# Kernel optimization log

Hardware: AMD Instinct MI355X
Metric: run time of the kernel (lower is better)

The kernel has to match this reference:

```python
import jax, jax.numpy as jnp
import numpy as np

D = 16          # input_dim (no augmentations)
HID = 256       # hidden_dim
WIN = 64        # window_size
LEN = 1000      # len_noise
INTU = 50       # len_interval_u
B = 512
PAIRS = D * (D - 1) // 2      # 120 depth-2 Lyndon pairs
LOGSIG = D + PAIRS            # 136 logsignature channels


def _static_schedule():
    """Replicates compute_multilevel_logsignature's index logic on static times."""
    tb = np.linspace(0.0, 1.0, LEN)
    tu = tb[::INTU]
    tt = np.linspace(0.0, 1.0, WIN)
    u_indices = np.searchsorted(tb, tu, side='right') - 1
    t_indices = np.searchsorted(tb, tt[1:], side='right') - 1
    u_idx_for_t = np.searchsorted(tu, tt[1:], side='right') - 1
    start_idx = u_indices[np.maximum(u_idx_for_t, 0)]
    # build u_logsigrnn times and the per-step last_h update mask
    qt, last = [], -1
    for iu in u_idx_for_t:
        iu = max(int(iu), 0)
        if iu != last:
            qt.append(tu[iu]); last = iu
    qt.append(tt[-1])
    upd = np.zeros(WIN, dtype=bool)
    for i, t in enumerate(tt):
        if qt and t >= qt[0]:
            qt.pop(0); upd[i] = True
    return tb, t_indices, start_idx, upd


def setup_inputs() -> dict:
    key = jax.random.key(0)
    ks = jax.random.split(key, 6)
    def lin(k, fo, fi):  # kaiming-style fan_in init
        return jax.random.normal(k, (fo, fi), jnp.float32) * np.float32(np.sqrt(2.0 / fi))
    return {
        "z": jax.random.normal(ks[0], (B, LEN, D), jnp.float32),
        "W1": lin(ks[1], HID, HID + LOGSIG), "b1": jnp.zeros((HID,), jnp.float32),
        "W2": lin(ks[2], HID, HID),          "b2": jnp.zeros((HID,), jnp.float32),
        "W3": lin(ks[3], HID, HID),          "b3": jnp.zeros((HID,), jnp.float32),
        "W_lin": lin(ks[4], HID, HID),
    }


def reference(z, W1, b1, W2, b2, W3, b3, W_lin):
    tb, t_idx, s_idx, upd = _static_schedule()
    # Brownian path: z[:,0]=0, z[:,1:] *= sqrt(dt), cumsum
    dt_sqrt = jnp.sqrt(jnp.asarray(np.diff(tb), jnp.float32))          # [LEN-1]
    z = jnp.concatenate([jnp.zeros_like(z[:, :1]), z[:, 1:] * dt_sqrt[None, :, None]], axis=1)
    X = jnp.cumsum(z, axis=1)                                           # [B,LEN,D]
    # depth-2 logsignature with basepoint=0: level1 = X[end]; level2 = Levy area
    iu, ju = np.triu_indices(D, 1)
    Xp, dX = X[:, :-1], X[:, 1:] - X[:, :-1]
    pair = Xp[..., iu] * dX[..., ju] - Xp[..., ju] * dX[..., iu]        # [B,LEN-1,PAIRS]
    C = jnp.concatenate([jnp.zeros_like(pair[:, :1]), jnp.cumsum(pair, axis=1)], axis=1)
    lvl1 = X[:, t_idx]
    levy = 0.5 * (C[:, t_idx] - C[:, s_idx])
    logsig = jnp.concatenate([lvl1, levy], axis=-1)
    logsig = jnp.concatenate([jnp.zeros_like(logsig[:, :1]), logsig], axis=1)  # prepend zeros
    seq = jnp.moveaxis(logsig, 1, 0)

    def mlp(v):  # FeedForwardNN([hid,hid]) + Tanh
        v = jax.nn.relu(v @ W1.T + b1)
        v = jax.nn.relu(v @ W2.T + b2)
        return jnp.tanh(v @ W3.T + b3)

    def step(last_h, xs):
        ls, u = xs
        h = mlp(jnp.concatenate([last_h, ls], axis=-1))
        new_last = jnp.where(u, h, last_h)
        return new_last, h @ W_lin.T

    h0 = jnp.zeros((z.shape[0], HID), z.dtype)  # init_fixed=True
    _, ys = jax.lax.scan(step, h0, (seq, jnp.asarray(upd)))
    return jnp.moveaxis(ys, 0, 1)
```

## Files before the change

### kernel.cpp

```cpp
#include <hip/hip_runtime.h>
#include <hip/hip_bf16.h>
#include <cmath>
#include <cstring>

#define B_SZ   512
#define SLEN   1000
#define DD     16
#define HID    256
#define WIN    64
#define PAIRS  120
#define LSIG   136
#define NWIN   20
#define MAXST  21
#define K1P    416
#define W1FN   (13 * 16 * 64 * 8)
#define WFN    (8 * 16 * 64 * 8)
#define PSTEP  21

using short8  = __attribute__((ext_vector_type(8))) short;
using short4v = __attribute__((ext_vector_type(4))) short;
using half8   = __attribute__((ext_vector_type(8))) _Float16;
using f32x4   = __attribute__((ext_vector_type(4))) float;

struct SchedArgs { short snapk[SLEN - 1]; };
struct CombPArgs { unsigned char winofm[WIN]; unsigned char zl[WIN]; unsigned char sstep[WIN]; };
struct ChainArgs { int nsteps; unsigned char kU[32]; };
struct FuseArgs  { unsigned char sidx[WIN]; };

__device__ __forceinline__ unsigned short f2h(float x) {
  _Float16 h = (_Float16)x;
  return __builtin_bit_cast(unsigned short, h);
}
__device__ __forceinline__ float ftanh(float x) {
  float t = fminf(fmaxf(2.f * x, -30.f), 30.f);
  float e = __expf(t);
  return (e - 1.f) / (e + 1.f);
}

__global__ __launch_bounds__(128) void prep_kernel(
    const float* __restrict__ z,
    const float* __restrict__ W1, const float* __restrict__ W2,
    const float* __restrict__ W3, const float* __restrict__ Wl,
    float* __restrict__ logsig, float* __restrict__ dxwin,
    unsigned short* __restrict__ W1f, unsigned short* __restrict__ W2f,
    unsigned short* __restrict__ W3f, unsigned short* __restrict__ Wlf,
    SchedArgs A)
{
  const int w = blockIdx.x, b = blockIdx.y, tid = threadIdx.x;
  if (w >= NWIN) {
    const int slot = ((w - NWIN) * B_SZ + b) * 128 + tid;
    for (int e = slot; e < W1FN + 3 * WFN; e += 3 * B_SZ * 128) {
      if (e < W1FN) {
        int f = e;
        int j = f & 7, l15 = (f >> 3) & 15, lq = (f >> 7) & 3, nsub = (f >> 9) & 15, kk = f >> 13;
        int row = nsub * 16 + l15, col = kk * 32 + lq * 8 + j;
        float v = (col < HID + LSIG) ? W1[(size_t)row * (HID + LSIG) + col] : 0.f;
        W1f[f] = f2h(v);
      } else {
        int e2 = e - W1FN;
        int which = e2 >> 16, f = e2 & 65535;
        int j = f & 7, l15 = (f >> 3) & 15, lq = (f >> 7) & 3, nsub = (f >> 9) & 15, kk = (f >> 13) & 7;
        int row = nsub * 16 + l15, col = kk * 32 + lq * 8 + j;
        const float* src = which == 0 ? W2 : which == 1 ? W3 : Wl;
        unsigned short* dst = which == 0 ? W2f : which == 1 ? W3f : Wlf;
        dst[f] = f2h(src[(size_t)row * HID + col]);
      }
    }
    return;
  }
  __shared__ float zs[50][16];
  const int ns = (w == NWIN - 1) ? 49 : 50;
  const float* src = z + ((size_t)b * SLEN + 50 * w + 1) * DD;
  const double s999 = 1.0 / (double)(SLEN - 1);
  for (int c = tid; c < ns * 4; c += 128) {
    float4 v = ((const float4*)src)[c];
    int t = 50 * w + (c >> 2);
    double a = (t + 1 == SLEN - 1) ? 1.0 : (double)(t + 1) * s999;
    float s = sqrtf((float)(a - (double)t * s999));
    v.x *= s; v.y *= s; v.z *= s; v.w *= s;
    ((float4*)&zs[0][0])[c] = v;
  }
  int pi = 0, pj = 0;
  if (tid < PAIRS) { int rem = tid, i = 0; while (rem >= DD - 1 - i) { rem -= DD - 1 - i; ++i; } pi = i; pj = i + 1 + rem; }
  __syncthreads();
  float Yi = 0.f, Yj = 0.f, LL = 0.f, Yd = 0.f;
  const int base_t = 50 * w;
  for (int u = 0; u < ns; ++u) {
    const float di = zs[u][pi], dj = zs[u][pj];
    LL = fmaf(Yi, dj, LL); LL = fmaf(-Yj, di, LL);
    Yi += di; Yj += dj;
    if (tid < DD) Yd += zs[u][tid];
    const int m = A.snapk[base_t + u];
    if (m) {
      float* dst = logsig + ((size_t)b * WIN + m) * LSIG;
      if (tid < DD)    dst[tid]      = Yd;
      if (tid < PAIRS) dst[DD + tid] = LL;
    }
  }
  if (tid < DD) dxwin[((size_t)b * NWIN + w) * DD + tid] = Yd;
}

__global__ __launch_bounds__(256) void combp_kernel(
    float* __restrict__ logsig, const float* __restrict__ dxwin,
    const unsigned short* __restrict__ W1f, const float* __restrict__ b1,
    float* __restrict__ partial, CombPArgs A)
{
  __shared__ float Xs[16][16], Yt[16][16];
  __shared__ __align__(16) unsigned short As[20 * 16 * 8];
  const int k = blockIdx.x, g = blockIdx.y, tid = threadIdx.x;
  const int w = A.winofm[k], zl = A.zl[k], ss = A.sstep[k];
  for (int c = tid; c < 3 * 16 * 8; c += 256) As[17 * 16 * 8 + c] = 0;
  {
    const int bi = tid >> 4, col = tid & 15;
    const size_t b = (size_t)(g * 16 + bi);
    float acc = 0.f;
    for (int ww = 0; ww < w; ++ww) acc += dxwin[(b * NWIN + ww) * DD + col];
    float y = (k == 0) ? 0.f : logsig[(b * WIN + k) * LSIG + col];
    float fin = (k == 0) ? 0.f : acc + y;
    Xs[bi][col] = acc; Yt[bi][col] = y;
    logsig[(b * WIN + k) * LSIG + col] = fin;
    As[((col >> 3) * 16 + bi) * 8 + (col & 7)] = f2h(fin);
  }
  __syncthreads();
  for (int idx = tid; idx < 16 * PAIRS; idx += 256) {
    const int bi = idx / PAIRS, p = idx - bi * PAIRS;
    int rem = p, i = 0; while (rem >= DD - 1 - i) { rem -= DD - 1 - i; ++i; }
    const int pi = i, pj = i + 1 + rem;
    const size_t b = (size_t)(g * 16 + bi);
    float ll = (k == 0) ? 0.f : logsig[(b * WIN + k) * LSIG + DD + p];
    float fin = (k == 0 || zl) ? 0.f
              : 0.5f * (ll + Xs[bi][pi] * Yt[bi][pj] - Xs[bi][pj] * Yt[bi][pi]);
    logsig[(b * WIN + k) * LSIG + DD + p] = fin;
    const int c = DD + p;
    As[((c >> 3) * 16 + bi) * 8 + (c & 7)] = f2h(fin);
  }
  if (ss == 255) return;
  __syncthreads();
  const int lane = tid & 63, wv = tid >> 6;
  const int l15 = lane & 15, lq = lane >> 4;
  f32x4 acc4[4] = {{0,0,0,0},{0,0,0,0},{0,0,0,0},{0,0,0,0}};
#pragma unroll
  for (int kt = 0; kt < 5; ++kt) {
    half8 af = *(const half8*)&As[((kt * 4 + lq) * 16 + l15) * 8];
#pragma unroll
    for (int t = 0; t < 4; ++t) {
      half8 bfW = *(const half8*)(W1f + ((size_t)((8 + kt) * 16 + wv * 4 + t) * 64 + lane) * 8);
      acc4[t] = __builtin_amdgcn_mfma_f32_16x16x32_f16(bfW, af, acc4[t], 0, 0, 0);
    }
  }
#pragma unroll
  for (int t = 0; t < 4; ++t) {
    const int col0 = wv * 64 + t * 16 + lq * 4;
    f32x4 bb = *(const f32x4*)(b1 + col0);
    f32x4 r = acc4[t] + bb;
    *(f32x4*)&partial[(((size_t)g * PSTEP + ss) * 16 + l15) * HID + col0] = r;
  }
}

__global__ __attribute__((amdgpu_flat_work_group_size(512, 512)))
__attribute__((amdgpu_waves_per_eu(2, 2)))
void chain_kernel(
    const float* __restrict__ partial,
    const unsigned short* __restrict__ W1f, const unsigned short* __restrict__ W2f,
    const unsigned short* __restrict__ W3f,
    const float* __restrict__ b2, const float* __restrict__ b3,
    unsigned short* __restrict__ statesb, ChainArgs A)
{
  __shared__ __align__(16) unsigned short A0s[32 * 16 * 8];
  __shared__ __align__(16) unsigned short A1s[32 * 16 * 8];
  __shared__ __align__(16) unsigned short A2s[32 * 16 * 8];
  const int tid = threadIdx.x, g = blockIdx.x;
  const int lane = tid & 63, w = tid >> 6;
  const int l15 = lane & 15, lq = lane >> 4;

  for (int c = tid; c < 32 * 16 * 8; c += 512) A0s[c] = 0;
  for (int c = tid; c < 16 * HID; c += 512) {
    int r = c >> 8, col = c & 255;
    statesb[((size_t)(g * 16 + r) * MAXST + 0) * HID + col] = 0;
  }

  half8 W1r[16], W2r[16], W3r[16];
#pragma unroll
  for (int kk = 0; kk < 8; ++kk)
#pragma unroll
    for (int nt = 0; nt < 2; ++nt) {
      W1r[kk * 2 + nt] = *(const half8*)(W1f + ((size_t)(kk * 16 + w * 2 + nt) * 64 + lane) * 8);
      W2r[kk * 2 + nt] = *(const half8*)(W2f + ((size_t)(kk * 16 + w * 2 + nt) * 64 + lane) * 8);
      W3r[kk * 2 + nt] = *(const half8*)(W3f + ((size_t)(kk * 16 + w * 2 + nt) * 64 + lane) * 8);
    }

  int colb[2];
  f32x4 bias2v[2], bias3v[2];
#pragma unroll
  for (int nt = 0; nt < 2; ++nt) {
    colb[nt] = w * 32 + nt * 16 + lq * 4;
    bias2v[nt] = *(const f32x4*)(b2 + colb[nt]);
    bias3v[nt] = *(const f32x4*)(b3 + colb[nt]);
  }

  const float* pbase = partial + (size_t)g * PSTEP * 16 * HID;
  int poff[2];
#pragma unroll
  for (int nt = 0; nt < 2; ++nt) poff[nt] = l15 * HID + colb[nt];
  f32x4 pf[2];
  pf[0] = *(const f32x4*)(pbase + poff[0]);
  pf[1] = *(const f32x4*)(pbase + poff[1]);

  short4v hv4[2];
  __syncthreads();

  for (int m = 0; m < A.nsteps; ++m) {
    if (m > 0) {
#pragma unroll
      for (int nt = 0; nt < 2; ++nt)
        *(short4v*)&statesb[((size_t)(g * 16 + l15) * MAXST + m) * HID + colb[nt]] = hv4[nt];
    }
    {
      f32x4 acc[2][2];
      acc[0][0] = pf[0]; acc[0][1] = pf[1];
      acc[1][0] = (f32x4){0.f,0.f,0.f,0.f}; acc[1][1] = (f32x4){0.f,0.f,0.f,0.f};
      if (m + 1 < A.nsteps) {
        const float* pp = pbase + (size_t)(m + 1) * 16 * HID;
        pf[0] = *(const f32x4*)(pp + poff[0]);
        pf[1] = *(const f32x4*)(pp + poff[1]);
      }
#pragma unroll
      for (int kk = 0; kk < 8; ++kk) {
        half8 af = *(const half8*)&A0s[((kk * 4 + lq) * 16 + l15) * 8];
        acc[kk & 1][0] = __builtin_amdgcn_mfma_f32_16x16x32_f16(W1r[kk * 2    ], af, acc[kk & 1][0], 0, 0, 0);
        acc[kk & 1][1] = __builtin_amdgcn_mfma_f32_16x16x32_f16(W1r[kk * 2 + 1], af, acc[kk & 1][1], 0, 0, 0);
      }
#pragma unroll
      for (int nt = 0; nt < 2; ++nt) {
        f32x4 s = acc[0][nt] + acc[1][nt];
        short4v h4;
#pragma unroll
        for (int r4 = 0; r4 < 4; ++r4) h4[r4] = (short)f2h(fmaxf(s[r4], 0.f));
        *(short4v*)&A1s[((colb[nt] >> 3) * 16 + l15) * 8 + (colb[nt] & 7)] = h4;
      }
    }
    __syncthreads();
    {
      f32x4 acc[2][2] = {{{0.f,0.f,0.f,0.f},{0.f,0.f,0.f,0.f}},{{0.f,0.f,0.f,0.f},{0.f,0.f,0.f,0.f}}};
#pragma unroll
      for (int kk = 0; kk < 8; ++kk) {
        half8 af = *(const half8*)&A1s[((kk * 4 + lq) * 16 + l15) * 8];
        acc[kk & 1][0] = __builtin_amdgcn_mfma_f32_16x16x32_f16(W2r[kk * 2    ], af, acc[kk & 1][0], 0, 0, 0);
        acc[kk & 1][1] = __builtin_amdgcn_mfma_f32_16x16x32_f16(W2r[kk * 2 + 1], af, acc[kk & 1][1], 0, 0, 0);
      }
#pragma unroll
      for (int nt = 0; nt < 2; ++nt) {
        f32x4 s = acc[0][nt] + acc[1][nt] + bias2v[nt];
        short4v h4;
#pragma unroll
        for (int r4 = 0; r4 < 4; ++r4) h4[r4] = (short)f2h(fmaxf(s[r4], 0.f));
        *(short4v*)&A2s[((colb[nt] >> 3) * 16 + l15) * 8 + (colb[nt] & 7)] = h4;
      }
    }
    __syncthreads();
    {
      f32x4 acc[2][2] = {{{0.f,0.f,0.f,0.f},{0.f,0.f,0.f,0.f}},{{0.f,0.f,0.f,0.f},{0.f,0.f,0.f,0.f}}};
#pragma unroll
      for (int kk = 0; kk < 8; ++kk) {
        half8 af = *(const half8*)&A2s[((kk * 4 + lq) * 16 + l15) * 8];
        acc[kk & 1][0] = __builtin_amdgcn_mfma_f32_16x16x32_f16(W3r[kk * 2    ], af, acc[kk & 1][0], 0, 0, 0);
        acc[kk & 1][1] = __builtin_amdgcn_mfma_f32_16x16x32_f16(W3r[kk * 2 + 1], af, acc[kk & 1][1], 0, 0, 0);
      }
#pragma unroll
      for (int nt = 0; nt < 2; ++nt) {
        f32x4 s = acc[0][nt] + acc[1][nt] + bias3v[nt];
        short4v h4;
#pragma unroll
        for (int r4 = 0; r4 < 4; ++r4) h4[r4] = (short)f2h(ftanh(s[r4]));
        hv4[nt] = h4;
        *(short4v*)&A0s[((colb[nt] >> 3) * 16 + l15) * 8 + (colb[nt] & 7)] = h4;
      }
    }
    __syncthreads();
  }
  {
    const int m = A.nsteps;
#pragma unroll
    for (int nt = 0; nt < 2; ++nt)
      *(short4v*)&statesb[((size_t)(g * 16 + l15) * MAXST + m) * HID + colb[nt]] = hv4[nt];
  }
}

__global__ __launch_bounds__(256, 4) void fused_kernel(
    const unsigned short* __restrict__ statesb, const float* __restrict__ logsig,
    const unsigned short* __restrict__ W1f, const unsigned short* __restrict__ W2f,
    const unsigned short* __restrict__ W3f, const unsigned short* __restrict__ Wlf,
    const float* __restrict__ b1, const float* __restrict__ b2, const float* __restrict__ b3,
    float* __restrict__ out, FuseArgs F)
{
  __shared__ __align__(16) unsigned short act[32 * 32 * 8];
  __shared__ __align__(16) unsigned short atile[2][4 * 32 * 8];
  const int tid = threadIdx.x;
  const int b = blockIdx.x >> 1, half = blockIdx.x & 1;
  const int lane = tid & 63, w = tid >> 6;
  const int l15 = lane & 15, lq = lane >> 4;

  f32x4 acc[2][4];
#pragma unroll
  for (int a = 0; a < 2; ++a)
#pragma unroll
    for (int t = 0; t < 4; ++t) acc[a][t] = (f32x4){0.f, 0.f, 0.f, 0.f};

  const int lr = tid >> 3, lcc = (tid & 7) * 4;
  const int lks = half * 32 + lr;
  short4v pk;
  auto loadA = [&](int kk) {
    int col = kk * 32 + lcc;
    if (col < HID) {
      pk = *(const short4v*)(statesb + ((size_t)b * MAXST + F.sidx[lks]) * HID + col);
    } else {
      const float* sp = logsig + ((size_t)b * WIN + lks) * LSIG + (col - HID);
      float4 v = *(const float4*)sp;
      short4v q;
      q[0] = (short)f2h(v.x); q[1] = (short)f2h(v.y); q[2] = (short)f2h(v.z); q[3] = (short)f2h(v.w);
      pk = q;
    }
  };
  loadA(0);
  for (int kk = 0; kk < 13; ++kk) {
    unsigned short* buf = &atile[kk & 1][0];
    *(short4v*)&buf[((lcc >> 3) * 32 + lr) * 8 + (lcc & 7)] = pk;
    __syncthreads();
    if (kk + 1 < 13) loadA(kk + 1);
    half8 bfr[4];
#pragma unroll
    for (int t = 0; t < 4; ++t)
      bfr[t] = *(const half8*)(W1f + ((size_t)(kk * 16 + w * 4 + t) * 64 + lane) * 8);
#pragma unroll
    for (int a = 0; a < 2; ++a) {
      half8 af = *(const half8*)&buf[(lq * 32 + a * 16 + l15) * 8];
#pragma unroll
      for (int t = 0; t < 4; ++t)
        acc[a][t] = __builtin_amdgcn_mfma_f32_16x16x32_f16(bfr[t], af, acc[a][t], 0, 0, 0);
    }
  }
#pragma unroll
  for (int t = 0; t < 4; ++t) {
    const int col0 = w * 64 + t * 16 + lq * 4;
    f32x4 bb = *(const f32x4*)(b1 + col0);
#pragma unroll
    for (int a = 0; a < 2; ++a) {
      const int row = a * 16 + l15;
      short4v h4;
#pragma unroll
      for (int r4 = 0; r4 < 4; ++r4) h4[r4] = (short)f2h(fmaxf(acc[a][t][r4] + bb[r4], 0.f));
      *(short4v*)&act[((col0 >> 3) * 32 + row) * 8 + (col0 & 7)] = h4;
    }
  }
  __syncthreads();

  auto layer = [&](const unsigned short* Wf) {
#pragma unroll
    for (int a = 0; a < 2; ++a)
#pragma unroll
      for (int t = 0; t < 4; ++t) acc[a][t] = (f32x4){0.f, 0.f, 0.f, 0.f};
    for (int kk = 0; kk < 8; ++kk) {
      half8 bfr[4];
#pragma unroll
      for (int t = 0; t < 4; ++t)
        bfr[t] = *(const half8*)(Wf + ((size_t)(kk * 16 + w * 4 + t) * 64 + lane) * 8);
#pragma unroll
      for (int a = 0; a < 2; ++a) {
        half8 af = *(const half8*)&act[((kk * 4 + lq) * 32 + a * 16 + l15) * 8];
#pragma unroll
        for (int t = 0; t < 4; ++t)
          acc[a][t] = __builtin_amdgcn_mfma_f32_16x16x32_f16(bfr[t], af, acc[a][t], 0, 0, 0);
      }
    }
  };

  layer(W2f);
  __syncthreads();
#pragma unroll
  for (int t = 0; t < 4; ++t) {
    const int col0 = w * 64 + t * 16 + lq * 4;
    f32x4 bb = *(const f32x4*)(b2 + col0);
#pragma unroll
    for (int a = 0; a < 2; ++a) {
      const int row = a * 16 + l15;
      short4v h4;
#pragma unroll
      for (int r4 = 0; r4 < 4; ++r4) h4[r4] = (short)f2h(fmaxf(acc[a][t][r4] + bb[r4], 0.f));
      *(short4v*)&act[((col0 >> 3) * 32 + row) * 8 + (col0 & 7)] = h4;
    }
  }
  __syncthreads();

  layer(W3f);
  __syncthreads();
#pragma unroll
  for (int t = 0; t < 4; ++t) {
    const int col0 = w * 64 + t * 16 + lq * 4;
    f32x4 bb = *(const f32x4*)(b3 + col0);
#pragma unroll
    for (int a = 0; a < 2; ++a) {
      const int row = a * 16 + l15;
      short4v h4;
#pragma unroll
      for (int r4 = 0; r4 < 4; ++r4) h4[r4] = (short)f2h(ftanh(acc[a][t][r4] + bb[r4]));
      *(short4v*)&act[((col0 >> 3) * 32 + row) * 8 + (col0 & 7)] = h4;
    }
  }
  __syncthreads();

  layer(Wlf);
#pragma unroll
  for (int t = 0; t < 4; ++t) {
    const int col0 = w * 64 + t * 16 + lq * 4;
#pragma unroll
    for (int a = 0; a < 2; ++a) {
      const int ks = half * 32 + a * 16 + l15;
      *(f32x4*)&out[((size_t)b * WIN + ks) * HID + col0] = acc[a][t];
    }
  }
}

static void build_sched(SchedArgs& P, CombPArgs& CB, ChainArgs& CH, FuseArgs& FU) {
  double tb[SLEN], tt[WIN], tu[NWIN];
  const double s999 = 1.0 / (double)(SLEN - 1);
  const double s63  = 1.0 / (double)(WIN - 1);
  for (int i = 0; i < SLEN; ++i) tb[i] = (double)i * s999;
  tb[SLEN - 1] = 1.0;
  for (int k = 0; k < WIN; ++k) tt[k] = (double)k * s63;
  tt[WIN - 1] = 1.0;
  for (int j = 0; j < NWIN; ++j) tu[j] = tb[50 * j];

  int t_idx[WIN - 1], u_for_t[WIN - 1];
  for (int k = 1; k < WIN; ++k) {
    int ii = 0;
    for (int q = 0; q < SLEN; ++q) if (tb[q] <= tt[k]) ii = q;
    t_idx[k - 1] = ii;
    int jj = 0;
    for (int q = 0; q < NWIN; ++q) if (tu[q] <= tt[k]) jj = q;
    u_for_t[k - 1] = jj;
  }
  for (int t = 0; t < SLEN - 1; ++t) P.snapk[t] = 0;
  for (int m = 1; m < WIN; ++m) P.snapk[t_idx[m - 1] - 1] = (short)m;

  for (int m = 0; m < WIN; ++m) { CB.winofm[m] = 0; CB.zl[m] = 0; CB.sstep[m] = 255; }
  for (int m = 1; m < WIN; ++m) {
    int p = t_idx[m - 1];
    CB.winofm[m] = (unsigned char)((p - 1) / 50);
    CB.zl[m] = (p % 50 == 0) ? 1 : 0;
  }

  double qt[32]; int nq = 0, last = -1;
  for (int m = 0; m < WIN - 1; ++m) {
    const int iu = u_for_t[m];
    if (iu != last) { qt[nq++] = tu[iu]; last = iu; }
  }
  qt[nq++] = tt[WIN - 1];
  int upd[WIN]; int qh = 0;
  for (int i = 0; i < WIN; ++i) {
    upd[i] = 0;
    if (qh < nq && tt[i] >= qt[qh]) { qh++; upd[i] = 1; }
  }
  int nU = 0;
  for (int k = 0; k < WIN; ++k) if (upd[k]) { if (nU < 32) CH.kU[nU] = (unsigned char)k; ++nU; }
  int cnt = 0;
  for (int k = 0; k < WIN; ++k) { FU.sidx[k] = (unsigned char)cnt; if (upd[k]) ++cnt; }
  CH.nsteps = FU.sidx[WIN - 1];
  for (int s = 0; s < nU && s < 32; ++s)
    if (s < PSTEP) CB.sstep[CH.kU[s]] = (unsigned char)s;
}

extern "C" void kernel_launch(void* const* d_in, const int* in_sizes, int n_in,
                              void* d_out, int out_size, void* d_ws, size_t ws_size,
                              hipStream_t stream) {
  const float* z  = (const float*)d_in[0];
  const float* W1 = (const float*)d_in[1];
  const float* b1 = (const float*)d_in[2];
  const float* W2 = (const float*)d_in[3];
  const float* b2 = (const float*)d_in[4];
  const float* W3 = (const float*)d_in[5];
  const float* b3 = (const float*)d_in[6];
  const float* Wl = (const float*)d_in[7];

  char* ws = (char*)d_ws;
  float* logsig = (float*)(ws);
  size_t o = (size_t)B_SZ * WIN * LSIG * 4;
  float* dxwin            = (float*)(ws + o); o += (size_t)B_SZ * NWIN * DD * 4;
  unsigned short* statesb = (unsigned short*)(ws + o); o += (size_t)B_SZ * MAXST * HID * 2;
  unsigned short* W1f     = (unsigned short*)(ws + o); o += (size_t)W1FN * 2;
  unsigned short* W2f     = (unsigned short*)(ws + o); o += (size_t)WFN * 2;
  unsigned short* W3f     = (unsigned short*)(ws + o); o += (size_t)WFN * 2;
  unsigned short* Wlf     = (unsigned short*)(ws + o); o += (size_t)WFN * 2;
  float* partial          = (float*)(ws + o); o += (size_t)32 * PSTEP * 16 * HID * 4;

  SchedArgs P; CombPArgs CB; ChainArgs CH; FuseArgs FU;
  build_sched(P, CB, CH, FU);

  prep_kernel<<<dim3(NWIN + 3, B_SZ), 128, 0, stream>>>(
      z, W1, W2, W3, Wl, logsig, dxwin, W1f, W2f, W3f, Wlf, P);
  combp_kernel<<<dim3(WIN, 32), 256, 0, stream>>>(logsig, dxwin, W1f, b1, partial, CB);
  chain_kernel<<<32, 512, 0, stream>>>(partial, W1f, W2f, W3f, b2, b3, statesb, CH);
  fused_kernel<<<1024, 256, 0, stream>>>(statesb, logsig, W1f, W2f, W3f, Wlf,
                                         b1, b2, b3, (float*)d_out, FU);
}
```

Before: 218.0 us.

## Halve chain-kernel waves and double fused-kernel rows per block

The sequential chain kernel drops from 8 to 4 waves per block, so each wave holds 4 N-tiles of all three weight matrices in registers. This cuts the number of waves meeting at each barrier, at the cost of more register pressure and more serial MFMA work per wave. The fused output kernel now handles all 64 window rows of one batch element per block (512 blocks instead of 1024), so each weight fragment loaded from global memory feeds four row tiles instead of two. It uses wider 8-element A-tile loads and larger shared buffers, trading occupancy (launch bounds lowered to 3) for better weight reuse.

```diff
diff --git a/kernel.cpp b/kernel.cpp
--- a/kernel.cpp
+++ b/kernel.cpp
@@ -157,8 +157,8 @@
   }
 }
 
-__global__ __attribute__((amdgpu_flat_work_group_size(512, 512)))
-__attribute__((amdgpu_waves_per_eu(2, 2)))
+__global__ __attribute__((amdgpu_flat_work_group_size(256, 256)))
+__attribute__((amdgpu_waves_per_eu(1, 1)))
 void chain_kernel(
     const float* __restrict__ partial,
     const unsigned short* __restrict__ W1f, const unsigned short* __restrict__ W2f,
@@ -173,84 +173,81 @@
   const int lane = tid & 63, w = tid >> 6;
   const int l15 = lane & 15, lq = lane >> 4;
 
-  for (int c = tid; c < 32 * 16 * 8; c += 512) A0s[c] = 0;
-  for (int c = tid; c < 16 * HID; c += 512) {
-    int r = c >> 8, col = c & 255;
-    statesb[((size_t)(g * 16 + r) * MAXST + 0) * HID + col] = 0;
-  }
-
-  half8 W1r[16], W2r[16], W3r[16];
+  for (int c = tid; c < 32 * 16 * 8; c += 256) A0s[c] = 0;
+  for (int c = tid; c < 16 * HID / 4; c += 256) {
+    int r = c >> 6, col = (c & 63) * 4;
+    *(short4v*)&statesb[((size_t)(g * 16 + r) * MAXST + 0) * HID + col] = (short4v){0, 0, 0, 0};
+  }
+
+  half8 W1r[8][4], W2r[8][4], W3r[8][4];
 #pragma unroll
   for (int kk = 0; kk < 8; ++kk)
 #pragma unroll
-    for (int nt = 0; nt < 2; ++nt) {
-      W1r[kk * 2 + nt] = *(const half8*)(W1f + ((size_t)(kk * 16 + w * 2 + nt) * 64 + lane) * 8);
-      W2r[kk * 2 + nt] = *(const half8*)(W2f + ((size_t)(kk * 16 + w * 2 + nt) * 64 + lane) * 8);
-      W3r[kk * 2 + nt] = *(const half8*)(W3f + ((size_t)(kk * 16 + w * 2 + nt) * 64 + lane) * 8);
-    }
-
-  int colb[2];
-  f32x4 bias2v[2], bias3v[2];
-#pragma unroll
-  for (int nt = 0; nt < 2; ++nt) {
-    colb[nt] = w * 32 + nt * 16 + lq * 4;
+    for (int nt = 0; nt < 4; ++nt) {
+      const size_t fo = ((size_t)(kk * 16 + w * 4 + nt) * 64 + lane) * 8;
+      W1r[kk][nt] = *(const half8*)(W1f + fo);
+      W2r[kk][nt] = *(const half8*)(W2f + fo);
+      W3r[kk][nt] = *(const half8*)(W3f + fo);
+    }
+
+  int colb[4];
+  f32x4 bias2v[4], bias3v[4];
+#pragma unroll
+  for (int nt = 0; nt < 4; ++nt) {
+    colb[nt] = w * 64 + nt * 16 + lq * 4;
     bias2v[nt] = *(const f32x4*)(b2 + colb[nt]);
     bias3v[nt] = *(const f32x4*)(b3 + colb[nt]);
   }
 
   const float* pbase = partial + (size_t)g * PSTEP * 16 * HID;
-  int poff[2];
-#pragma unroll
-  for (int nt = 0; nt < 2; ++nt) poff[nt] = l15 * HID + colb[nt];
-  f32x4 pf[2];
-  pf[0] = *(const f32x4*)(pbase + poff[0]);
-  pf[1] = *(const f32x4*)(pbase + poff[1]);
-
-  short4v hv4[2];
+  f32x4 pf[4];
+#pragma unroll
+  for (int nt = 0; nt < 4; ++nt) pf[nt] = *(const f32x4*)(pbase + l15 * HID + colb[nt]);
+
+  short4v hv4[4];
   __syncthreads();
 
   for (int m = 0; m < A.nsteps; ++m) {
     if (m > 0) {
 #pragma unroll
-      for (int nt = 0; nt < 2; ++nt)
+      for (int nt = 0; nt < 4; ++nt)
         *(short4v*)&statesb[((size_t)(g * 16 + l15) * MAXST + m) * HID + colb[nt]] = hv4[nt];
     }
     {
-      f32x4 acc[2][2];
-      acc[0][0] = pf[0]; acc[0][1] = pf[1];
-      acc[1][0] = (f32x4){0.f,0.f,0.f,0.f}; acc[1][1] = (f32x4){0.f,0.f,0.f,0.f};
+      f32x4 acc[4] = {pf[0], pf[1], pf[2], pf[3]};
       if (m + 1 < A.nsteps) {
         const float* pp = pbase + (size_t)(m + 1) * 16 * HID;
-        pf[0] = *(const f32x4*)(pp + poff[0]);
-        pf[1] = *(const f32x4*)(pp + poff[1]);
+#pragma unroll
+        for (int nt = 0; nt < 4; ++nt) pf[nt] = *(const f32x4*)(pp + l15 * HID + colb[nt]);
       }
 #pragma unroll
       for (int kk = 0; kk < 8; ++kk) {
         half8 af = *(const half8*)&A0s[((kk * 4 + lq) * 16 + l15) * 8];
-        acc[kk & 1][0] = __builtin_amdgcn_mfma_f32_16x16x32_f16(W1r[kk * 2    ], af, acc[kk & 1][0], 0, 0, 0);
-        acc[kk & 1][1] = __builtin_amdgcn_mfma_f32_16x16x32_f16(W1r[kk * 2 + 1], af, acc[kk & 1][1], 0, 0, 0);
-      }
-#pragma unroll
-      for (int nt = 0; nt < 2; ++nt) {
-        f32x4 s = acc[0][nt] + acc[1][nt];
+#pragma unroll
+        for (int nt = 0; nt < 4; ++nt)
+          acc[nt] = __builtin_amdgcn_mfma_f32_16x16x32_f16(W1r[kk][nt], af, acc[nt], 0, 0, 0);
+      }
+#pragma unroll
+      for (int nt = 0; nt < 4; ++nt) {
         short4v h4;
 #pragma unroll
-        for (int r4 = 0; r4 < 4; ++r4) h4[r4] = (short)f2h(fmaxf(s[r4], 0.f));
+        for (int r4 = 0; r4 < 4; ++r4) h4[r4] = (short)f2h(fmaxf(acc[nt][r4], 0.f));
         *(short4v*)&A1s[((colb[nt] >> 3) * 16 + l15) * 8 + (colb[nt] & 7)] = h4;
       }
     }
     __syncthreads();
     {
-      f32x4 acc[2][2] = {{{0.f,0.f,0.f,0.f},{0.f,0.f,0.f,0.f}},{{0.f,0.f,0.f,0.f},{0.f,0.f,0.f,0.f}}};
+      f32x4 acc[4] = {{0.f,0.f,0.f,0.f},{0.f,0.f,0.f,0.f},{0.f,0.f,0.f,0.f},{0.f,0.f,0.f,0.f}};
 #pragma unroll
       for (int kk = 0; kk < 8; ++kk) {
         half8 af = *(const half8*)&A1s[((kk * 4 + lq) * 16 + l15) * 8];
-        acc[kk & 1][0] = __builtin_amdgcn_mfma_f32_16x16x32_f16(W2r[kk * 2    ], af, acc[kk & 1][0], 0, 0, 0);
-        acc[kk & 1][1] = __builtin_amdgcn_mfma_f32_16x16x32_f16(W2r[kk * 2 + 1], af, acc[kk & 1][1], 0, 0, 0);
-      }
-#pragma unroll
-      for (int nt = 0; nt < 2; ++nt) {
-        f32x4 s = acc[0][nt] + acc[1][nt] + bias2v[nt];
+#pragma unroll
+        for (int nt = 0; nt < 4; ++nt)
+          acc[nt] = __builtin_amdgcn_mfma_f32_16x16x32_f16(W2r[kk][nt], af, acc[nt], 0, 0, 0);
+      }
+#pragma unroll
+      for (int nt = 0; nt < 4; ++nt) {
+        f32x4 s = acc[nt] + bias2v[nt];
         short4v h4;
 #pragma unroll
         for (int r4 = 0; r4 < 4; ++r4) h4[r4] = (short)f2h(fmaxf(s[r4], 0.f));
@@ -259,16 +256,17 @@
     }
     __syncthreads();
     {
-      f32x4 acc[2][2] = {{{0.f,0.f,0.f,0.f},{0.f,0.f,0.f,0.f}},{{0.f,0.f,0.f,0.f},{0.f,0.f,0.f,0.f}}};
+      f32x4 acc[4] = {{0.f,0.f,0.f,0.f},{0.f,0.f,0.f,0.f},{0.f,0.f,0.f,0.f},{0.f,0.f,0.f,0.f}};
 #pragma unroll
       for (int kk = 0; kk < 8; ++kk) {
         half8 af = *(const half8*)&A2s[((kk * 4 + lq) * 16 + l15) * 8];
-        acc[kk & 1][0] = __builtin_amdgcn_mfma_f32_16x16x32_f16(W3r[kk * 2    ], af, acc[kk & 1][0], 0, 0, 0);
-        acc[kk & 1][1] = __builtin_amdgcn_mfma_f32_16x16x32_f16(W3r[kk * 2 + 1], af, acc[kk & 1][1], 0, 0, 0);
-      }
-#pragma unroll
-      for (int nt = 0; nt < 2; ++nt) {
-        f32x4 s = acc[0][nt] + acc[1][nt] + bias3v[nt];
+#pragma unroll
+        for (int nt = 0; nt < 4; ++nt)
+          acc[nt] = __builtin_amdgcn_mfma_f32_16x16x32_f16(W3r[kk][nt], af, acc[nt], 0, 0, 0);
+      }
+#pragma unroll
+      for (int nt = 0; nt < 4; ++nt) {
+        f32x4 s = acc[nt] + bias3v[nt];
         short4v h4;
 #pragma unroll
         for (int r4 = 0; r4 < 4; ++r4) h4[r4] = (short)f2h(ftanh(s[r4]));
@@ -281,50 +279,50 @@
   {
     const int m = A.nsteps;
 #pragma unroll
-    for (int nt = 0; nt < 2; ++nt)
+    for (int nt = 0; nt < 4; ++nt)
       *(short4v*)&statesb[((size_t)(g * 16 + l15) * MAXST + m) * HID + colb[nt]] = hv4[nt];
   }
 }
 
-__global__ __launch_bounds__(256, 4) void fused_kernel(
+__global__ __launch_bounds__(256, 3) void fused_kernel(
     const unsigned short* __restrict__ statesb, const float* __restrict__ logsig,
     const unsigned short* __restrict__ W1f, const unsigned short* __restrict__ W2f,
     const unsigned short* __restrict__ W3f, const unsigned short* __restrict__ Wlf,
     const float* __restrict__ b1, const float* __restrict__ b2, const float* __restrict__ b3,
     float* __restrict__ out, FuseArgs F)
 {
-  __shared__ __align__(16) unsigned short act[32 * 32 * 8];
-  __shared__ __align__(16) unsigned short atile[2][4 * 32 * 8];
-  const int tid = threadIdx.x;
-  const int b = blockIdx.x >> 1, half = blockIdx.x & 1;
+  __shared__ __align__(16) unsigned short act[32 * 64 * 8];
+  __shared__ __align__(16) unsigned short atile[2][4 * 64 * 8];
+  const int tid = threadIdx.x, b = blockIdx.x;
   const int lane = tid & 63, w = tid >> 6;
   const int l15 = lane & 15, lq = lane >> 4;
 
-  f32x4 acc[2][4];
-#pragma unroll
-  for (int a = 0; a < 2; ++a)
+  f32x4 acc[4][4];
+#pragma unroll
+  for (int a = 0; a < 4; ++a)
 #pragma unroll
     for (int t = 0; t < 4; ++t) acc[a][t] = (f32x4){0.f, 0.f, 0.f, 0.f};
 
-  const int lr = tid >> 3, lcc = (tid & 7) * 4;
-  const int lks = half * 32 + lr;
-  short4v pk;
+  const int lr = tid >> 2, lcc = (tid & 3) * 8;
+  short8 pk;
   auto loadA = [&](int kk) {
     int col = kk * 32 + lcc;
     if (col < HID) {
-      pk = *(const short4v*)(statesb + ((size_t)b * MAXST + F.sidx[lks]) * HID + col);
+      pk = *(const short8*)(statesb + ((size_t)b * MAXST + F.sidx[lr]) * HID + col);
     } else {
-      const float* sp = logsig + ((size_t)b * WIN + lks) * LSIG + (col - HID);
-      float4 v = *(const float4*)sp;
-      short4v q;
-      q[0] = (short)f2h(v.x); q[1] = (short)f2h(v.y); q[2] = (short)f2h(v.z); q[3] = (short)f2h(v.w);
+      const float* sp = logsig + ((size_t)b * WIN + lr) * LSIG + (col - HID);
+      float4 v0 = ((const float4*)sp)[0];
+      float4 v1 = ((const float4*)sp)[1];
+      short8 q;
+      q[0] = (short)f2h(v0.x); q[1] = (short)f2h(v0.y); q[2] = (short)f2h(v0.z); q[3] = (short)f2h(v0.w);
+      q[4] = (short)f2h(v1.x); q[5] = (short)f2h(v1.y); q[6] = (short)f2h(v1.z); q[7] = (short)f2h(v1.w);
       pk = q;
     }
   };
   loadA(0);
   for (int kk = 0; kk < 13; ++kk) {
     unsigned short* buf = &atile[kk & 1][0];
-    *(short4v*)&buf[((lcc >> 3) * 32 + lr) * 8 + (lcc & 7)] = pk;
+    *(short8*)&buf[((lcc >> 3) * 64 + lr) * 8] = pk;
     __syncthreads();
     if (kk + 1 < 13) loadA(kk + 1);
     half8 bfr[4];
@@ -332,8 +330,8 @@
     for (int t = 0; t < 4; ++t)
       bfr[t] = *(const half8*)(W1f + ((size_t)(kk * 16 + w * 4 + t) * 64 + lane) * 8);
 #pragma unroll
-    for (int a = 0; a < 2; ++a) {
-      half8 af = *(const half8*)&buf[(lq * 32 + a * 16 + l15) * 8];
+    for (int a = 0; a < 4; ++a) {
+      half8 af = *(const half8*)&buf[(lq * 64 + a * 16 + l15) * 8];
 #pragma unroll
       for (int t = 0; t < 4; ++t)
         acc[a][t] = __builtin_amdgcn_mfma_f32_16x16x32_f16(bfr[t], af, acc[a][t], 0, 0, 0);
@@ -344,19 +342,19 @@
     const int col0 = w * 64 + t * 16 + lq * 4;
     f32x4 bb = *(const f32x4*)(b1 + col0);
 #pragma unroll
-    for (int a = 0; a < 2; ++a) {
+    for (int a = 0; a < 4; ++a) {
       const int row = a * 16 + l15;
       short4v h4;
 #pragma unroll
       for (int r4 = 0; r4 < 4; ++r4) h4[r4] = (short)f2h(fmaxf(acc[a][t][r4] + bb[r4], 0.f));
-      *(short4v*)&act[((col0 >> 3) * 32 + row) * 8 + (col0 & 7)] = h4;
+      *(short4v*)&act[((col0 >> 3) * 64 + row) * 8 + (col0 & 7)] = h4;
     }
   }
   __syncthreads();
 
   auto layer = [&](const unsigned short* Wf) {
 #pragma unroll
-    for (int a = 0; a < 2; ++a)
+    for (int a = 0; a < 4; ++a)
 #pragma unroll
       for (int t = 0; t < 4; ++t) acc[a][t] = (f32x4){0.f, 0.f, 0.f, 0.f};
     for (int kk = 0; kk < 8; ++kk) {
@@ -365,8 +363,8 @@
       for (int t = 0; t < 4; ++t)
         bfr[t] = *(const half8*)(Wf + ((size_t)(kk * 16 + w * 4 + t) * 64 + lane) * 8);
 #pragma unroll
-      for (int a = 0; a < 2; ++a) {
-        half8 af = *(const half8*)&act[((kk * 4 + lq) * 32 + a * 16 + l15) * 8];
+      for (int a = 0; a < 4; ++a) {
+        half8 af = *(const half8*)&act[((kk * 4 + lq) * 64 + a * 16 + l15) * 8];
 #pragma unroll
         for (int t = 0; t < 4; ++t)
           acc[a][t] = __builtin_amdgcn_mfma_f32_16x16x32_f16(bfr[t], af, acc[a][t], 0, 0, 0);
@@ -381,12 +379,12 @@
     const int col0 = w * 64 + t * 16 + lq * 4;
     f32x4 bb = *(const f32x4*)(b2 + col0);
 #pragma unroll
-    for (int a = 0; a < 2; ++a) {
+    for (int a = 0; a < 4; ++a) {
       const int row = a * 16 + l15;
       short4v h4;
 #pragma unroll
       for (int r4 = 0; r4 < 4; ++r4) h4[r4] = (short)f2h(fmaxf(acc[a][t][r4] + bb[r4], 0.f));
-      *(short4v*)&act[((col0 >> 3) * 32 + row) * 8 + (col0 & 7)] = h4;
+      *(short4v*)&act[((col0 >> 3) * 64 + row) * 8 + (col0 & 7)] = h4;
     }
   }
   __syncthreads();
@@ -398,12 +396,12 @@
     const int col0 = w * 64 + t * 16 + lq * 4;
     f32x4 bb = *(const f32x4*)(b3 + col0);
 #pragma unroll
-    for (int a = 0; a < 2; ++a) {
+    for (int a = 0; a < 4; ++a) {
       const int row = a * 16 + l15;
       short4v h4;
 #pragma unroll
       for (int r4 = 0; r4 < 4; ++r4) h4[r4] = (short)f2h(ftanh(acc[a][t][r4] + bb[r4]));
-      *(short4v*)&act[((col0 >> 3) * 32 + row) * 8 + (col0 & 7)] = h4;
+      *(short4v*)&act[((col0 >> 3) * 64 + row) * 8 + (col0 & 7)] = h4;
     }
   }
   __syncthreads();
@@ -413,8 +411,8 @@
   for (int t = 0; t < 4; ++t) {
     const int col0 = w * 64 + t * 16 + lq * 4;
 #pragma unroll
-    for (int a = 0; a < 2; ++a) {
-      const int ks = half * 32 + a * 16 + l15;
+    for (int a = 0; a < 4; ++a) {
+      const int ks = a * 16 + l15;
       *(f32x4*)&out[((size_t)b * WIN + ks) * HID + col0] = acc[a][t];
     }
   }
@@ -498,7 +496,7 @@
   prep_kernel<<<dim3(NWIN + 3, B_SZ), 128, 0, stream>>>(
       z, W1, W2, W3, Wl, logsig, dxwin, W1f, W2f, W3f, Wlf, P);
   combp_kernel<<<dim3(WIN, 32), 256, 0, stream>>>(logsig, dxwin, W1f, b1, partial, CB);
-  chain_kernel<<<32, 512, 0, stream>>>(partial, W1f, W2f, W3f, b2, b3, statesb, CH);
-  fused_kernel<<<1024, 256, 0, stream>>>(statesb, logsig, W1f, W2f, W3f, Wlf,
-                                         b1, b2, b3, (float*)d_out, FU);
-}
+  chain_kernel<<<32, 256, 0, stream>>>(partial, W1f, W2f, W3f, b2, b3, statesb, CH);
+  fused_kernel<<<512, 256, 0, stream>>>(statesb, logsig, W1f, W2f, W3f, Wlf,
+                                        b1, b2, b3, (float*)d_out, FU);
+}
```

New measurement: 239.6 us. 9.9% more time.

## Merge combine and chain kernels with per-step flag handoff

Applied to the files above, without the earlier changes.

Fuses the logsignature-combine/partial-GEMM kernel and the recurrent chain kernel into one launch. Chain blocks spin on per-(group,step) flags that combine blocks set after writing their partial products, so the chain can start while later partials are still being computed. This removes a kernel boundary and overlaps the combine work with the serial chain. The risk is deadlock or stalls if chain blocks occupy CUs before the combine blocks they wait on are scheduled, and the spin waits and fences add latency to each step.

```diff
diff --git a/kernel.cpp b/kernel.cpp
--- a/kernel.cpp
+++ b/kernel.cpp
@@ -44,10 +44,12 @@
     float* __restrict__ logsig, float* __restrict__ dxwin,
     unsigned short* __restrict__ W1f, unsigned short* __restrict__ W2f,
     unsigned short* __restrict__ W3f, unsigned short* __restrict__ Wlf,
-    SchedArgs A)
+    int* __restrict__ flags, SchedArgs A)
 {
   const int w = blockIdx.x, b = blockIdx.y, tid = threadIdx.x;
   if (w >= NWIN) {
+    if (w == NWIN && b == 0)
+      for (int c = tid; c < 32 * PSTEP; c += 128) flags[c] = 0;
     const int slot = ((w - NWIN) * B_SZ + b) * 128 + tid;
     for (int e = slot; e < W1FN + 3 * WFN; e += 3 * B_SZ * 128) {
       if (e < W1FN) {
@@ -100,83 +102,90 @@
   if (tid < DD) dxwin[((size_t)b * NWIN + w) * DD + tid] = Yd;
 }
 
-__global__ __launch_bounds__(256) void combp_kernel(
-    float* __restrict__ logsig, const float* __restrict__ dxwin,
-    const unsigned short* __restrict__ W1f, const float* __restrict__ b1,
-    float* __restrict__ partial, CombPArgs A)
-{
-  __shared__ float Xs[16][16], Yt[16][16];
-  __shared__ __align__(16) unsigned short As[20 * 16 * 8];
-  const int k = blockIdx.x, g = blockIdx.y, tid = threadIdx.x;
-  const int w = A.winofm[k], zl = A.zl[k], ss = A.sstep[k];
-  for (int c = tid; c < 3 * 16 * 8; c += 256) As[17 * 16 * 8 + c] = 0;
-  {
-    const int bi = tid >> 4, col = tid & 15;
-    const size_t b = (size_t)(g * 16 + bi);
-    float acc = 0.f;
-    for (int ww = 0; ww < w; ++ww) acc += dxwin[(b * NWIN + ww) * DD + col];
-    float y = (k == 0) ? 0.f : logsig[(b * WIN + k) * LSIG + col];
-    float fin = (k == 0) ? 0.f : acc + y;
-    Xs[bi][col] = acc; Yt[bi][col] = y;
-    logsig[(b * WIN + k) * LSIG + col] = fin;
-    As[((col >> 3) * 16 + bi) * 8 + (col & 7)] = f2h(fin);
-  }
-  __syncthreads();
-  for (int idx = tid; idx < 16 * PAIRS; idx += 256) {
-    const int bi = idx / PAIRS, p = idx - bi * PAIRS;
-    int rem = p, i = 0; while (rem >= DD - 1 - i) { rem -= DD - 1 - i; ++i; }
-    const int pi = i, pj = i + 1 + rem;
-    const size_t b = (size_t)(g * 16 + bi);
-    float ll = (k == 0) ? 0.f : logsig[(b * WIN + k) * LSIG + DD + p];
-    float fin = (k == 0 || zl) ? 0.f
-              : 0.5f * (ll + Xs[bi][pi] * Yt[bi][pj] - Xs[bi][pj] * Yt[bi][pi]);
-    logsig[(b * WIN + k) * LSIG + DD + p] = fin;
-    const int c = DD + p;
-    As[((c >> 3) * 16 + bi) * 8 + (c & 7)] = f2h(fin);
-  }
-  if (ss == 255) return;
-  __syncthreads();
-  const int lane = tid & 63, wv = tid >> 6;
-  const int l15 = lane & 15, lq = lane >> 4;
-  f32x4 acc4[4] = {{0,0,0,0},{0,0,0,0},{0,0,0,0},{0,0,0,0}};
-#pragma unroll
-  for (int kt = 0; kt < 5; ++kt) {
-    half8 af = *(const half8*)&As[((kt * 4 + lq) * 16 + l15) * 8];
-#pragma unroll
-    for (int t = 0; t < 4; ++t) {
-      half8 bfW = *(const half8*)(W1f + ((size_t)((8 + kt) * 16 + wv * 4 + t) * 64 + lane) * 8);
-      acc4[t] = __builtin_amdgcn_mfma_f32_16x16x32_f16(bfW, af, acc4[t], 0, 0, 0);
-    }
-  }
-#pragma unroll
-  for (int t = 0; t < 4; ++t) {
-    const int col0 = wv * 64 + t * 16 + lq * 4;
-    f32x4 bb = *(const f32x4*)(b1 + col0);
-    f32x4 r = acc4[t] + bb;
-    *(f32x4*)&partial[(((size_t)g * PSTEP + ss) * 16 + l15) * HID + col0] = r;
-  }
-}
-
 __global__ __attribute__((amdgpu_flat_work_group_size(512, 512)))
 __attribute__((amdgpu_waves_per_eu(2, 2)))
-void chain_kernel(
-    const float* __restrict__ partial,
+void combchain_kernel(
+    float* __restrict__ logsig, const float* __restrict__ dxwin,
     const unsigned short* __restrict__ W1f, const unsigned short* __restrict__ W2f,
     const unsigned short* __restrict__ W3f,
-    const float* __restrict__ b2, const float* __restrict__ b3,
-    unsigned short* __restrict__ statesb, ChainArgs A)
+    const float* __restrict__ b1, const float* __restrict__ b2, const float* __restrict__ b3,
+    unsigned short* __restrict__ statesb, float* __restrict__ partial,
+    int* __restrict__ flags, CombPArgs CB, ChainArgs A)
 {
   __shared__ __align__(16) unsigned short A0s[32 * 16 * 8];
   __shared__ __align__(16) unsigned short A1s[32 * 16 * 8];
   __shared__ __align__(16) unsigned short A2s[32 * 16 * 8];
-  const int tid = threadIdx.x, g = blockIdx.x;
+  const int tid = threadIdx.x, bid = blockIdx.x;
+
+  if (bid >= 32) {
+    const int cb = bid - 32;
+    const int g = cb & 31, k = cb >> 5;
+    const int w = CB.winofm[k], zl = CB.zl[k], ss = CB.sstep[k];
+    float* Xs = (float*)A0s;
+    float* Yt = Xs + 256;
+    unsigned short* As = A1s;
+    for (int c = tid; c < 3 * 16 * 8; c += 512) As[17 * 16 * 8 + c] = 0;
+    if (tid < 256) {
+      const int bi = tid >> 4, col = tid & 15;
+      const size_t b = (size_t)(g * 16 + bi);
+      float acc = 0.f;
+      for (int ww = 0; ww < w; ++ww) acc += dxwin[(b * NWIN + ww) * DD + col];
+      float y = (k == 0) ? 0.f : logsig[(b * WIN + k) * LSIG + col];
+      float fin = (k == 0) ? 0.f : acc + y;
+      Xs[bi * 16 + col] = acc; Yt[bi * 16 + col] = y;
+      logsig[(b * WIN + k) * LSIG + col] = fin;
+      As[((col >> 3) * 16 + bi) * 8 + (col & 7)] = f2h(fin);
+    }
+    __syncthreads();
+    for (int idx = tid; idx < 16 * PAIRS; idx += 512) {
+      const int bi = idx / PAIRS, p = idx - bi * PAIRS;
+      int rem = p, i = 0; while (rem >= DD - 1 - i) { rem -= DD - 1 - i; ++i; }
+      const int pi = i, pj = i + 1 + rem;
+      const size_t b = (size_t)(g * 16 + bi);
+      float ll = (k == 0) ? 0.f : logsig[(b * WIN + k) * LSIG + DD + p];
+      float fin = (k == 0 || zl) ? 0.f
+                : 0.5f * (ll + Xs[bi * 16 + pi] * Yt[bi * 16 + pj] - Xs[bi * 16 + pj] * Yt[bi * 16 + pi]);
+      logsig[(b * WIN + k) * LSIG + DD + p] = fin;
+      const int c = DD + p;
+      As[((c >> 3) * 16 + bi) * 8 + (c & 7)] = f2h(fin);
+    }
+    if (ss == 255) return;
+    __syncthreads();
+    if (tid < 256) {
+      const int lane = tid & 63, wv = tid >> 6;
+      const int l15 = lane & 15, lq = lane >> 4;
+      f32x4 acc4[4] = {{0,0,0,0},{0,0,0,0},{0,0,0,0},{0,0,0,0}};
+#pragma unroll
+      for (int kt = 0; kt < 5; ++kt) {
+        half8 af = *(const half8*)&As[((kt * 4 + lq) * 16 + l15) * 8];
+#pragma unroll
+        for (int t = 0; t < 4; ++t) {
+          half8 bfW = *(const half8*)(W1f + ((size_t)((8 + kt) * 16 + wv * 4 + t) * 64 + lane) * 8);
+          acc4[t] = __builtin_amdgcn_mfma_f32_16x16x32_f16(bfW, af, acc4[t], 0, 0, 0);
+        }
+      }
+#pragma unroll
+      for (int t = 0; t < 4; ++t) {
+        const int col0 = wv * 64 + t * 16 + lq * 4;
+        f32x4 bb = *(const f32x4*)(b1 + col0);
+        f32x4 r = acc4[t] + bb;
+        *(f32x4*)&partial[(((size_t)g * PSTEP + ss) * 16 + l15) * HID + col0] = r;
+      }
+    }
+    __threadfence();
+    __syncthreads();
+    if (tid == 0) atomicExch(&flags[g * PSTEP + ss], 1);
+    return;
+  }
+
+  const int g = bid;
   const int lane = tid & 63, w = tid >> 6;
   const int l15 = lane & 15, lq = lane >> 4;
 
   for (int c = tid; c < 32 * 16 * 8; c += 512) A0s[c] = 0;
-  for (int c = tid; c < 16 * HID; c += 512) {
-    int r = c >> 8, col = c & 255;
-    statesb[((size_t)(g * 16 + r) * MAXST + 0) * HID + col] = 0;
+  for (int c = tid; c < 16 * HID / 4; c += 512) {
+    int r = c >> 6, col = (c & 63) * 4;
+    *(short4v*)&statesb[((size_t)(g * 16 + r) * MAXST + 0) * HID + col] = (short4v){0, 0, 0, 0};
   }
 
   half8 W1r[16], W2r[16], W3r[16];
@@ -202,12 +211,20 @@
   int poff[2];
 #pragma unroll
   for (int nt = 0; nt < 2; ++nt) poff[nt] = l15 * HID + colb[nt];
+
+  if (tid == 0) {
+    while (atomicAdd(&flags[g * PSTEP + 0], 0) == 0) __builtin_amdgcn_s_sleep(8);
+    if (1 < A.nsteps)
+      while (atomicAdd(&flags[g * PSTEP + 1], 0) == 0) __builtin_amdgcn_s_sleep(8);
+    __threadfence();
+  }
+  __syncthreads();
+
   f32x4 pf[2];
   pf[0] = *(const f32x4*)(pbase + poff[0]);
   pf[1] = *(const f32x4*)(pbase + poff[1]);
 
   short4v hv4[2];
-  __syncthreads();
 
   for (int m = 0; m < A.nsteps; ++m) {
     if (m > 0) {
@@ -275,6 +292,10 @@
         hv4[nt] = h4;
         *(short4v*)&A0s[((colb[nt] >> 3) * 16 + l15) * 8 + (colb[nt] & 7)] = h4;
       }
+    }
+    if (tid == 0 && m + 2 < A.nsteps) {
+      while (atomicAdd(&flags[g * PSTEP + m + 2], 0) == 0) __builtin_amdgcn_s_sleep(8);
+      __threadfence();
     }
     __syncthreads();
   }
@@ -491,14 +512,15 @@
   unsigned short* W3f     = (unsigned short*)(ws + o); o += (size_t)WFN * 2;
   unsigned short* Wlf     = (unsigned short*)(ws + o); o += (size_t)WFN * 2;
   float* partial          = (float*)(ws + o); o += (size_t)32 * PSTEP * 16 * HID * 4;
+  int* flags              = (int*)(ws + o);   o += (size_t)32 * PSTEP * 4;
 
   SchedArgs P; CombPArgs CB; ChainArgs CH; FuseArgs FU;
   build_sched(P, CB, CH, FU);
 
   prep_kernel<<<dim3(NWIN + 3, B_SZ), 128, 0, stream>>>(
-      z, W1, W2, W3, Wl, logsig, dxwin, W1f, W2f, W3f, Wlf, P);
-  combp_kernel<<<dim3(WIN, 32), 256, 0, stream>>>(logsig, dxwin, W1f, b1, partial, CB);
-  chain_kernel<<<32, 512, 0, stream>>>(partial, W1f, W2f, W3f, b2, b3, statesb, CH);
+      z, W1, W2, W3, Wl, logsig, dxwin, W1f, W2f, W3f, Wlf, flags, P);
+  combchain_kernel<<<32 + WIN * 32, 512, 0, stream>>>(
+      logsig, dxwin, W1f, W2f, W3f, b1, b2, b3, statesb, partial, flags, CB, CH);
   fused_kernel<<<1024, 256, 0, stream>>>(statesb, logsig, W1f, W2f, W3f, Wlf,
                                          b1, b2, b3, (float*)d_out, FU);
 }
```

Result: slower. 360.1 us (+65.2%).
